# Kernel optimization log

Measured on AMD Instinct MI355X. Metric: run time of the kernel, lower is better.

## Reference

```python
import jax, jax.numpy as jnp
import numpy as np

D = 512
NHEAD = 8
BLOCK = 256
N = 131072
DFF = 2 * D
EPS = 1e-5


def _layernorm(x, g, b):
    mu = jnp.mean(x, axis=-1, keepdims=True)
    var = jnp.mean((x - mu) ** 2, axis=-1, keepdims=True)
    return (x - mu) * jax.lax.rsqrt(var + EPS) * g + b


def setup_inputs() -> dict:
    key = jax.random.key(0)
    ks = jax.random.split(key, 6)
    s = 0.02
    return {
        "x": jax.random.normal(ks[0], (N, D), jnp.float32),
        "in_proj_w": jax.random.normal(ks[1], (3 * D, D), jnp.float32) * s,
        "in_proj_b": jnp.zeros((3 * D,), jnp.float32),
        "out_w": jax.random.normal(ks[2], (D, D), jnp.float32) * s,
        "out_b": jnp.zeros((D,), jnp.float32),
        "lin1_w": jax.random.normal(ks[3], (DFF, D), jnp.float32) * s,
        "lin1_b": jnp.zeros((DFF,), jnp.float32),
        "lin2_w": jax.random.normal(ks[4], (D, DFF), jnp.float32) * s,
        "lin2_b": jnp.zeros((D,), jnp.float32),
        "ln1_g": jnp.ones((D,), jnp.float32),
        "ln1_beta": jnp.zeros((D,), jnp.float32),
        "ln2_g": jnp.ones((D,), jnp.float32),
        "ln2_beta": jnp.zeros((D,), jnp.float32),
        "block_size": BLOCK,
    }


def reference(x, in_proj_w, in_proj_b, out_w, out_b, lin1_w, lin1_b,
              lin2_w, lin2_b, ln1_g, ln1_beta, ln2_g, ln2_beta, block_size):
    n, d = x.shape
    nb = n // block_size  # N divisible by block_size -> equal chunks
    hd = d // NHEAD
    xb = x.reshape(nb, block_size, d)  # [B,S,D], each block independent

    # --- Multi-head self-attention (per block, batched) ---
    qkv = jnp.einsum('bsd,ed->bse', xb, in_proj_w) + in_proj_b  # [B,S,3D]
    q, k, v = jnp.split(qkv, 3, axis=-1)
    q = q.reshape(nb, block_size, NHEAD, hd)
    k = k.reshape(nb, block_size, NHEAD, hd)
    v = v.reshape(nb, block_size, NHEAD, hd)
    scores = jnp.einsum('bshd,bthd->bhst', q, k) / jnp.sqrt(jnp.float32(hd))
    probs = jax.nn.softmax(scores, axis=-1)
    ctx = jnp.einsum('bhst,bthd->bshd', probs, v).reshape(nb, block_size, d)
    attn_out = jnp.einsum('bsd,ed->bse', ctx, out_w) + out_b

    # post-norm residuals (torch default norm_first=False)
    h = _layernorm(xb + attn_out, ln1_g, ln1_beta)

    # --- FFN with exact-erf gelu ---
    ff = jnp.einsum('bsd,fd->bsf', h, lin1_w) + lin1_b
    ff = jax.nn.gelu(ff, approximate=False)
    ff = jnp.einsum('bsf,df->bsd', ff, lin2_w) + lin2_b
    out = _layernorm(h + ff, ln2_g, ln2_beta)
    return out.reshape(n, d)
```

## Files before the change

kernel.cpp:

```cpp
#include <hip/hip_runtime.h>
#include <hip/hip_bf16.h>
#include <math.h>

#define NTOK 131072
#define DMODEL 512
#define DFF_ 1024
#define NHEAD 8
#define HD 64
#define BLK 256
#define NB (NTOK / BLK)

typedef __hip_bfloat16 bf16;

__device__ __forceinline__ float bf_to_f(unsigned short u) {
    return __uint_as_float(((unsigned)u) << 16);
}
__device__ __forceinline__ unsigned short f_to_bf(float f) {
    bf16 h = __float2bfloat16(f);
    return __builtin_bit_cast(unsigned short, h);
}

typedef __bf16 bfrag __attribute__((ext_vector_type(8)));
typedef float f4t __attribute__((ext_vector_type(4)));

__device__ __forceinline__ float loadR(const float* p) { return *p; }
__device__ __forceinline__ float loadR(const ushort* p) { return bf_to_f(*p); }
__device__ __forceinline__ void storeC(float* p, float v) { *p = v; }
__device__ __forceinline__ void storeC(ushort* p, float v) { *p = f_to_bf(v); }

#define GLD_LDS(g, l)                                        \
    __builtin_amdgcn_global_load_lds(                        \
        (const __attribute__((address_space(1))) void*)(g),  \
        (__attribute__((address_space(3))) void*)(l), 16, 0, 0)

template <typename TO, typename TR, bool RESID, bool DO_GELU>
__global__ __launch_bounds__(256) void gemm_bf16(const ushort* __restrict__ A,
                                                 const ushort* __restrict__ B,
                                                 const float* __restrict__ bias,
                                                 const TR* __restrict__ resid,
                                                 TO* __restrict__ C,
                                                 int M, int Nn, int K) {
    __shared__ __align__(16) ushort As[128 * 64];
    __shared__ __align__(16) ushort Bs[128 * 64];

    const int tid = threadIdx.x;
    const int lane = tid & 63;
    const int w = tid >> 6;
    const int wm = w >> 1, wn = w & 1;

    const int ntn = Nn >> 7;
    int wg = blockIdx.x;
    const int cpx = (int)gridDim.x >> 3;
    wg = (wg & 7) * cpx + (wg >> 3);
    const int m0 = (wg / ntn) << 7;
    const int n0 = (wg % ntn) << 7;

    const int lr8 = lane >> 3;
    const int gsc = (lane & 7) << 3;

    const ushort* pa[4];
    const ushort* pb[4];
    ushort* la[4];
    ushort* lb[4];
#pragma unroll
    for (int i = 0; i < 4; ++i) {
        const int chunk = (w << 2) + i;
        const int r = (chunk << 3) + lr8;
        pa[i] = A + (size_t)(m0 + r) * K + gsc;
        pb[i] = B + (size_t)(n0 + r) * K + gsc;
        la[i] = As + (chunk << 9);
        lb[i] = Bs + (chunk << 9);
    }

    f4t zz = {0.f, 0.f, 0.f, 0.f};
    f4t acc[4][4];
#pragma unroll
    for (int i = 0; i < 4; ++i)
#pragma unroll
        for (int j = 0; j < 4; ++j) acc[i][j] = zz;

    const int fr = lane & 15;
    const int kq = lane >> 4;

    for (int kt = 0; kt < K; kt += 64) {
#pragma unroll
        for (int i = 0; i < 4; ++i) {
            GLD_LDS(pa[i], la[i]);
            GLD_LDS(pb[i], lb[i]);
            pa[i] += 64;
            pb[i] += 64;
        }
        __syncthreads();
#pragma unroll
        for (int ks = 0; ks < 2; ++ks) {
            const int sg = ((ks << 2) + kq) << 3;
            bfrag av[4], bv[4];
#pragma unroll
            for (int f = 0; f < 4; ++f) {
                av[f] = *(const bfrag*)(As + (((wm << 6) + (f << 4) + fr) << 6) + sg);
                bv[f] = *(const bfrag*)(Bs + (((wn << 6) + (f << 4) + fr) << 6) + sg);
            }
#pragma unroll
            for (int fm = 0; fm < 4; ++fm)
#pragma unroll
                for (int fn = 0; fn < 4; ++fn)
                    acc[fm][fn] = __builtin_amdgcn_mfma_f32_16x16x32_bf16(
                        av[fm], bv[fn], acc[fm][fn], 0, 0, 0);
        }
        __syncthreads();
    }

#pragma unroll
    for (int fn = 0; fn < 4; ++fn) {
        const int col = n0 + (wn << 6) + (fn << 4) + fr;
        const float bs = bias[col];
#pragma unroll
        for (int fm = 0; fm < 4; ++fm) {
            const int rw = m0 + (wm << 6) + (fm << 4) + (kq << 2);
#pragma unroll
            for (int j = 0; j < 4; ++j) {
                float v = acc[fm][fn][j] + bs;
                const size_t off = (size_t)(rw + j) * Nn + col;
                if constexpr (RESID) v += loadR(resid + off);
                if constexpr (DO_GELU)
                    v = 0.5f * v * (1.f + erff(v * 0.70710678118654752f));
                storeC(C + off, v);
            }
        }
    }
}

__global__ __launch_bounds__(256, 1) void attn_mfma(const ushort* __restrict__ qkv,
                                                    ushort* __restrict__ ctx) {
    __shared__ __align__(16) ushort Ks[256][72];
    __shared__ __align__(16) ushort Vt[64][264];
    __shared__ __align__(16) ushort Pl[4][64][40];
    const int b = blockIdx.x >> 3;
    const int h = blockIdx.x & 7;
    const int t = threadIdx.x;
    const int lane = t & 63;
    const int w = t >> 6;
    const int fr = lane & 15;
    const int kq = lane >> 4;

    {
        const ushort* rowp = qkv + (size_t)(b * BLK + t) * 1536 + h * HD;
#pragma unroll
        for (int c = 0; c < 8; ++c) {
            uint4 kv = *(const uint4*)(rowp + DMODEL + c * 8);
            *(uint4*)&Ks[t][c * 8] = kv;
            union { uint4 u; ushort s[8]; } vv;
            vv.u = *(const uint4*)(rowp + 2 * DMODEL + c * 8);
#pragma unroll
            for (int e = 0; e < 8; ++e) Vt[c * 8 + e][t] = vv.s[e];
        }
    }

    bfrag qb[4][2];
#pragma unroll
    for (int fn = 0; fn < 4; ++fn) {
        const ushort* qp =
            qkv + (size_t)(b * BLK + (w << 6) + (fn << 4) + fr) * 1536 + h * HD;
#pragma unroll
        for (int ks = 0; ks < 2; ++ks)
            qb[fn][ks] = *(const bfrag*)(qp + (ks << 5) + (kq << 3));
    }
    __syncthreads();

    f4t zz = {0.f, 0.f, 0.f, 0.f};
    f4t o[4][4];
#pragma unroll
    for (int i = 0; i < 4; ++i)
#pragma unroll
        for (int j = 0; j < 4; ++j) o[i][j] = zz;
    float m[4] = {-1e30f, -1e30f, -1e30f, -1e30f};
    float l[4] = {0.f, 0.f, 0.f, 0.f};

    for (int kt = 0; kt < 4; ++kt) {
        f4t s[4][4];
#pragma unroll
        for (int i = 0; i < 4; ++i)
#pragma unroll
            for (int j = 0; j < 4; ++j) s[i][j] = zz;
#pragma unroll
        for (int ks = 0; ks < 2; ++ks) {
            bfrag ka[4];
#pragma unroll
            for (int fm = 0; fm < 4; ++fm)
                ka[fm] = *(const bfrag*)&Ks[(kt << 6) + (fm << 4) + fr][(ks << 5) + (kq << 3)];
#pragma unroll
            for (int fm = 0; fm < 4; ++fm)
#pragma unroll
                for (int fn = 0; fn < 4; ++fn)
                    s[fm][fn] = __builtin_amdgcn_mfma_f32_16x16x32_bf16(
                        ka[fm], qb[fn][ks], s[fm][fn], 0, 0, 0);
        }
#pragma unroll
        for (int fn = 0; fn < 4; ++fn) {
            float mx = -1e30f;
#pragma unroll
            for (int fm = 0; fm < 4; ++fm)
#pragma unroll
                for (int j = 0; j < 4; ++j) {
                    float v = s[fm][fn][j] * 0.125f;
                    s[fm][fn][j] = v;
                    mx = fmaxf(mx, v);
                }
            mx = fmaxf(mx, __shfl_xor(mx, 16));
            mx = fmaxf(mx, __shfl_xor(mx, 32));
            const float mn = fmaxf(m[fn], mx);
            const float corr = __expf(m[fn] - mn);
            m[fn] = mn;
            l[fn] *= corr;
#pragma unroll
            for (int fm = 0; fm < 4; ++fm)
#pragma unroll
                for (int j = 0; j < 4; ++j) o[fm][fn][j] *= corr;
            float ps = 0.f;
#pragma unroll
            for (int fm = 0; fm < 4; ++fm)
#pragma unroll
                for (int j = 0; j < 4; ++j) {
                    float p = __expf(s[fm][fn][j] - mn);
                    s[fm][fn][j] = p;
                    ps += p;
                }
            l[fn] += ps;
        }
#pragma unroll
        for (int fn = 0; fn < 4; ++fn)
#pragma unroll
            for (int fm = 0; fm < 4; ++fm)
#pragma unroll
                for (int jj = 0; jj < 2; ++jj) {
                    unsigned u = (unsigned)f_to_bf(s[fm][fn][2 * jj]) |
                                 ((unsigned)f_to_bf(s[fm][fn][2 * jj + 1]) << 16);
                    *(unsigned*)&Pl[w][(fn << 4) + fr][(fm << 4) + (kq << 2) + 2 * jj] = u;
                }
#pragma unroll
        for (int c = 0; c < 2; ++c) {
            bfrag va[4], pb[4];
#pragma unroll
            for (int fm = 0; fm < 4; ++fm)
                va[fm] = *(const bfrag*)&Vt[(fm << 4) + fr][(kt << 6) + (c << 5) + (kq << 3)];
#pragma unroll
            for (int fn = 0; fn < 4; ++fn)
                pb[fn] = *(const bfrag*)&Pl[w][(fn << 4) + fr][(c << 5) + (kq << 3)];
#pragma unroll
            for (int fm = 0; fm < 4; ++fm)
#pragma unroll
                for (int fn = 0; fn < 4; ++fn)
                    o[fm][fn] = __builtin_amdgcn_mfma_f32_16x16x32_bf16(
                        va[fm], pb[fn], o[fm][fn], 0, 0, 0);
        }
    }

    float linv[4];
#pragma unroll
    for (int fn = 0; fn < 4; ++fn) {
        float ls = l[fn];
        ls += __shfl_xor(ls, 16);
        ls += __shfl_xor(ls, 32);
        linv[fn] = 1.f / ls;
    }
#pragma unroll
    for (int fn = 0; fn < 4; ++fn) {
        const size_t qg = (size_t)(b * BLK + (w << 6) + (fn << 4) + fr);
#pragma unroll
        for (int fm = 0; fm < 4; ++fm) {
            ushort4 ov;
            ov.x = f_to_bf(o[fm][fn][0] * linv[fn]);
            ov.y = f_to_bf(o[fm][fn][1] * linv[fn]);
            ov.z = f_to_bf(o[fm][fn][2] * linv[fn]);
            ov.w = f_to_bf(o[fm][fn][3] * linv[fn]);
            *(ushort4*)(ctx + qg * DMODEL + h * HD + (fm << 4) + (kq << 2)) = ov;
        }
    }
}

template <bool WF, bool WB>
__global__ __launch_bounds__(256) void ln_rows2(const float* __restrict__ in,
                                                float* __restrict__ outf,
                                                ushort* __restrict__ outb,
                                                const float* __restrict__ gg,
                                                const float* __restrict__ bb) {
    const int lane = threadIdx.x & 63;
    const int wv = threadIdx.x >> 6;
    const size_t row = (size_t)blockIdx.x * 4 + wv;
    const float* p = in + row * DMODEL + lane * 8;
    float4 a = ((const float4*)p)[0];
    float4 c = ((const float4*)p)[1];
    float s = a.x + a.y + a.z + a.w + c.x + c.y + c.z + c.w;
    float ss = a.x * a.x + a.y * a.y + a.z * a.z + a.w * a.w +
               c.x * c.x + c.y * c.y + c.z * c.z + c.w * c.w;
#pragma unroll
    for (int off = 1; off < 64; off <<= 1) {
        s += __shfl_xor(s, off, 64);
        ss += __shfl_xor(ss, off, 64);
    }
    const float mu = s * (1.f / 512.f);
    const float var = ss * (1.f / 512.f) - mu * mu;
    const float rstd = 1.f / sqrtf(var + 1e-5f);
    const int c0 = lane * 8;
    float4 g0 = *(const float4*)(gg + c0), g1 = *(const float4*)(gg + c0 + 4);
    float4 b0 = *(const float4*)(bb + c0), b1 = *(const float4*)(bb + c0 + 4);
    float4 o0, o1;
    o0.x = (a.x - mu) * rstd * g0.x + b0.x;
    o0.y = (a.y - mu) * rstd * g0.y + b0.y;
    o0.z = (a.z - mu) * rstd * g0.z + b0.z;
    o0.w = (a.w - mu) * rstd * g0.w + b0.w;
    o1.x = (c.x - mu) * rstd * g1.x + b1.x;
    o1.y = (c.y - mu) * rstd * g1.y + b1.y;
    o1.z = (c.z - mu) * rstd * g1.z + b1.z;
    o1.w = (c.w - mu) * rstd * g1.w + b1.w;
    if constexpr (WF) {
        float* qp = outf + row * DMODEL + c0;
        ((float4*)qp)[0] = o0;
        ((float4*)qp)[1] = o1;
    }
    if constexpr (WB) {
        ushort* bp = outb + row * DMODEL + c0;
        ushort4 u0, u1;
        u0.x = f_to_bf(o0.x); u0.y = f_to_bf(o0.y);
        u0.z = f_to_bf(o0.z); u0.w = f_to_bf(o0.w);
        u1.x = f_to_bf(o1.x); u1.y = f_to_bf(o1.y);
        u1.z = f_to_bf(o1.z); u1.w = f_to_bf(o1.w);
        ((ushort4*)bp)[0] = u0;
        ((ushort4*)bp)[1] = u1;
    }
}

__global__ __launch_bounds__(256) void cvt_f32_bf16(const float* __restrict__ in,
                                                    ushort* __restrict__ out,
                                                    int n4) {
    int i = blockIdx.x * 256 + threadIdx.x;
    const int stride = gridDim.x * 256;
    for (; i < n4; i += stride) {
        float4 v = ((const float4*)in)[i];
        ushort4 o;
        o.x = f_to_bf(v.x); o.y = f_to_bf(v.y);
        o.z = f_to_bf(v.z); o.w = f_to_bf(v.w);
        ((ushort4*)out)[i] = o;
    }
}

extern "C" void kernel_launch(void* const* d_in, const int* in_sizes, int n_in,
                              void* d_out, int out_size, void* d_ws, size_t ws_size,
                              hipStream_t stream) {
    const float* x    = (const float*)d_in[0];
    const float* wqkv = (const float*)d_in[1];
    const float* bqkv = (const float*)d_in[2];
    const float* wo   = (const float*)d_in[3];
    const float* bo   = (const float*)d_in[4];
    const float* w1   = (const float*)d_in[5];
    const float* b1   = (const float*)d_in[6];
    const float* w2   = (const float*)d_in[7];
    const float* b2   = (const float*)d_in[8];
    const float* g1   = (const float*)d_in[9];
    const float* be1  = (const float*)d_in[10];
    const float* g2   = (const float*)d_in[11];
    const float* be2  = (const float*)d_in[12];
    float* out = (float*)d_out;

    const size_t MiB = 1ull << 20;
    char* ws = (char*)d_ws;
    char* ob = (char*)d_out;
    const bool roomy = ws_size >= 520 * MiB;

    ushort* qkv = (ushort*)ws;
    float*  h   = (float*)ws;
    ushort* hb  = (ushort*)(ws + 256 * MiB);
    ushort* ctx = (ushort*)ob;

    ushort *wqkvb, *wob, *w1b, *w2b, *xb, *ff;
    float* y2;
    if (roomy) {
        wqkvb = (ushort*)(ws + 512 * MiB);
        wob   = (ushort*)(ws + 514 * MiB);
        w1b   = (ushort*)(ws + 515 * MiB);
        w2b   = (ushort*)(ws + 516 * MiB);
        xb    = (ushort*)(ws + 384 * MiB);
        ff    = (ushort*)ob;
        y2    = (float*)(ws + 256 * MiB);
    } else {
        wqkvb = (ushort*)(ws + 384 * MiB);
        wob   = (ushort*)(ws + 386 * MiB);
        w1b   = (ushort*)(ws + 387 * MiB);
        w2b   = (ushort*)(ws + 388 * MiB);
        xb    = (ushort*)ob;
        ff    = (ushort*)ws;
        y2    = (float*)ob;
    }

    dim3 blk(256);
    auto cvt = [&](const float* src, ushort* dst, size_t n) {
        int n4 = (int)(n >> 2);
        int nb = (n4 + 255) / 256;
        if (nb > 4096) nb = 4096;
        cvt_f32_bf16<<<dim3(nb), blk, 0, stream>>>(src, dst, n4);
    };
    cvt(x, xb, (size_t)NTOK * DMODEL);
    cvt(wqkv, wqkvb, 1536 * 512);
    cvt(wo, wob, 512 * 512);
    cvt(w1, w1b, 1024 * 512);
    cvt(w2, w2b, 512 * 1024);

    gemm_bf16<ushort, float, false, false><<<dim3(12 * 1024), blk, 0, stream>>>(
        xb, wqkvb, bqkv, (const float*)nullptr, qkv, NTOK, 1536, 512);
    attn_mfma<<<dim3(NB * NHEAD), blk, 0, stream>>>(qkv, ctx);
    gemm_bf16<float, float, true, false><<<dim3(4 * 1024), blk, 0, stream>>>(
        ctx, wob, bo, x, h, NTOK, 512, 512);
    if (roomy)
        ln_rows2<true, true><<<dim3(NTOK / 4), blk, 0, stream>>>(h, h, hb, g1, be1);
    else
        ln_rows2<false, true><<<dim3(NTOK / 4), blk, 0, stream>>>(h, nullptr, hb, g1, be1);
    gemm_bf16<ushort, float, false, true><<<dim3(8 * 1024), blk, 0, stream>>>(
        hb, w1b, b1, (const float*)nullptr, ff, NTOK, 1024, 512);
    if (roomy)
        gemm_bf16<float, float, true, false><<<dim3(4 * 1024), blk, 0, stream>>>(
            ff, w2b, b2, h, y2, NTOK, 512, 1024);
    else
        gemm_bf16<float, ushort, true, false><<<dim3(4 * 1024), blk, 0, stream>>>(
            ff, w2b, b2, hb, y2, NTOK, 512, 1024);
    ln_rows2<true, false><<<dim3(NTOK / 4), blk, 0, stream>>>(y2, out, nullptr, g2, be2);
}
```

Before: 2.150 ms.

## Replace GEMM with 256x256 tiles, double-buffered LDS and XOR-swizzled loads

The bf16 GEMM becomes a 512-thread, 256x256-tile kernel. Global-to-LDS loads for the next K tile are double-buffered and interleaved with MFMA work, using explicit waitcnt and barriers, raised wave priority around the MFMAs, and an XOR swizzle on the LDS layout to avoid bank conflicts. The host side drops the workspace-size branch and always uses the compact buffer layout, so the second residual is read from the bf16 h copy. The larger tiles increase register and LDS use per block, which can cap occupancy.

Result: faster. 1.808 ms (-15.9%).

```diff
diff --git a/kernel.cpp b/kernel.cpp
--- a/kernel.cpp
+++ b/kernel.cpp
@@ -34,80 +34,97 @@
         (__attribute__((address_space(3))) void*)(l), 16, 0, 0)
 
 template <typename TO, typename TR, bool RESID, bool DO_GELU>
-__global__ __launch_bounds__(256) void gemm_bf16(const ushort* __restrict__ A,
+__global__ __launch_bounds__(512, 2) void gemm8p(const ushort* __restrict__ A,
                                                  const ushort* __restrict__ B,
                                                  const float* __restrict__ bias,
                                                  const TR* __restrict__ resid,
                                                  TO* __restrict__ C,
                                                  int M, int Nn, int K) {
-    __shared__ __align__(16) ushort As[128 * 64];
-    __shared__ __align__(16) ushort Bs[128 * 64];
+    __shared__ __align__(16) ushort Ls[2][2][2][128][64];
 
     const int tid = threadIdx.x;
     const int lane = tid & 63;
     const int w = tid >> 6;
-    const int wm = w >> 1, wn = w & 1;
-
-    const int ntn = Nn >> 7;
+    const int wm = w >> 2;
+    const int wn = w & 3;
+    const int fr = lane & 15;
+    const int kq = lane >> 4;
+    const int sr = lane >> 3;
+    const int su = (lane & 7) ^ sr;
+
+    const int ntn = Nn >> 8;
     int wg = blockIdx.x;
     const int cpx = (int)gridDim.x >> 3;
     wg = (wg & 7) * cpx + (wg >> 3);
-    const int m0 = (wg / ntn) << 7;
-    const int n0 = (wg % ntn) << 7;
-
-    const int lr8 = lane >> 3;
-    const int gsc = (lane & 7) << 3;
-
-    const ushort* pa[4];
-    const ushort* pb[4];
-    ushort* la[4];
-    ushort* lb[4];
-#pragma unroll
-    for (int i = 0; i < 4; ++i) {
-        const int chunk = (w << 2) + i;
-        const int r = (chunk << 3) + lr8;
-        pa[i] = A + (size_t)(m0 + r) * K + gsc;
-        pb[i] = B + (size_t)(n0 + r) * K + gsc;
-        la[i] = As + (chunk << 9);
-        lb[i] = Bs + (chunk << 9);
-    }
+    const int m0 = (wg / ntn) << 8;
+    const int n0 = (wg % ntn) << 8;
+
+    auto stage_ht = [&](int db, int mat, int t, int h) {
+#pragma unroll
+        for (int i = 0; i < 2; ++i) {
+            const int seg = (w << 1) + i;
+            const int rr = (h << 7) + (seg << 3) + sr;
+            const ushort* gp = (mat ? B : A) +
+                (size_t)((mat ? n0 : m0) + rr) * K + (t << 6) + (su << 3);
+            GLD_LDS(gp, &Ls[db][mat][h][seg << 3][0]);
+        }
+    };
 
     f4t zz = {0.f, 0.f, 0.f, 0.f};
-    f4t acc[4][4];
-#pragma unroll
-    for (int i = 0; i < 4; ++i)
+    f4t acc[8][4];
+#pragma unroll
+    for (int i = 0; i < 8; ++i)
 #pragma unroll
         for (int j = 0; j < 4; ++j) acc[i][j] = zz;
 
-    const int fr = lane & 15;
-    const int kq = lane >> 4;
-
-    for (int kt = 0; kt < K; kt += 64) {
-#pragma unroll
-        for (int i = 0; i < 4; ++i) {
-            GLD_LDS(pa[i], la[i]);
-            GLD_LDS(pb[i], lb[i]);
-            pa[i] += 64;
-            pb[i] += 64;
-        }
-        __syncthreads();
-#pragma unroll
-        for (int ks = 0; ks < 2; ++ks) {
-            const int sg = ((ks << 2) + kq) << 3;
+    const int NT = K >> 6;
+    stage_ht(0, 0, 0, 0); stage_ht(0, 0, 0, 1);
+    stage_ht(0, 1, 0, 0); stage_ht(0, 1, 0, 1);
+
+    for (int tt = 0; tt < NT; tt += 2) {
+#pragma unroll
+        for (int p = 0; p < 8; ++p) {
+            const int hi = p >> 2;
+            const int q = p & 3;
+            const int mh = q & 1;
+            const int ks = q >> 1;
+            const int dc = hi;
+            const int ds_ = 1 - hi;
+            const int st = tt + 1 + hi;
+            const bool do_stage = st < NT;
+
+            if (q == 0) {
+                if (do_stage) {
+                    stage_ht(ds_, 0, st, 0);
+                    asm volatile("s_waitcnt vmcnt(2)\n\ts_barrier" ::: "memory");
+                } else {
+                    asm volatile("s_waitcnt vmcnt(0)\n\ts_barrier" ::: "memory");
+                }
+            }
+
             bfrag av[4], bv[4];
+            const int uu = ((((ks << 2) | kq)) ^ (fr & 7)) << 3;
 #pragma unroll
             for (int f = 0; f < 4; ++f) {
-                av[f] = *(const bfrag*)(As + (((wm << 6) + (f << 4) + fr) << 6) + sg);
-                bv[f] = *(const bfrag*)(Bs + (((wn << 6) + (f << 4) + fr) << 6) + sg);
+                const int rA = (wm << 7) + (mh << 6) + (f << 4) + fr;
+                av[f] = *(const bfrag*)&Ls[dc][0][rA >> 7][rA & 127][uu];
+                const int rB = (wn << 6) + (f << 4) + fr;
+                bv[f] = *(const bfrag*)&Ls[dc][1][rB >> 7][rB & 127][uu];
             }
-#pragma unroll
-            for (int fm = 0; fm < 4; ++fm)
+            if (q != 0 && do_stage) {
+                stage_ht(ds_, q >> 1, st, q & 1);
+            }
+
+            __builtin_amdgcn_s_setprio(1);
+#pragma unroll
+            for (int f = 0; f < 4; ++f)
 #pragma unroll
                 for (int fn = 0; fn < 4; ++fn)
-                    acc[fm][fn] = __builtin_amdgcn_mfma_f32_16x16x32_bf16(
-                        av[fm], bv[fn], acc[fm][fn], 0, 0, 0);
-        }
-        __syncthreads();
+                    acc[(mh << 2) + f][fn] = __builtin_amdgcn_mfma_f32_16x16x32_bf16(
+                        av[f], bv[fn], acc[(mh << 2) + f][fn], 0, 0, 0);
+            __builtin_amdgcn_s_setprio(0);
+            __builtin_amdgcn_s_barrier();
+        }
     }
 
 #pragma unroll
@@ -115,8 +132,8 @@
         const int col = n0 + (wn << 6) + (fn << 4) + fr;
         const float bs = bias[col];
 #pragma unroll
-        for (int fm = 0; fm < 4; ++fm) {
-            const int rw = m0 + (wm << 6) + (fm << 4) + (kq << 2);
+        for (int fm = 0; fm < 8; ++fm) {
+            const int rw = m0 + (wm << 7) + (fm << 4) + (kq << 2);
 #pragma unroll
             for (int j = 0; j < 4; ++j) {
                 float v = acc[fm][fn][j] + bs;
@@ -365,39 +382,25 @@
     const size_t MiB = 1ull << 20;
     char* ws = (char*)d_ws;
     char* ob = (char*)d_out;
-    const bool roomy = ws_size >= 520 * MiB;
-
-    ushort* qkv = (ushort*)ws;
-    float*  h   = (float*)ws;
-    ushort* hb  = (ushort*)(ws + 256 * MiB);
-    ushort* ctx = (ushort*)ob;
-
-    ushort *wqkvb, *wob, *w1b, *w2b, *xb, *ff;
-    float* y2;
-    if (roomy) {
-        wqkvb = (ushort*)(ws + 512 * MiB);
-        wob   = (ushort*)(ws + 514 * MiB);
-        w1b   = (ushort*)(ws + 515 * MiB);
-        w2b   = (ushort*)(ws + 516 * MiB);
-        xb    = (ushort*)(ws + 384 * MiB);
-        ff    = (ushort*)ob;
-        y2    = (float*)(ws + 256 * MiB);
-    } else {
-        wqkvb = (ushort*)(ws + 384 * MiB);
-        wob   = (ushort*)(ws + 386 * MiB);
-        w1b   = (ushort*)(ws + 387 * MiB);
-        w2b   = (ushort*)(ws + 388 * MiB);
-        xb    = (ushort*)ob;
-        ff    = (ushort*)ws;
-        y2    = (float*)ob;
-    }
-
-    dim3 blk(256);
+
+    ushort* qkv   = (ushort*)ws;
+    float*  h     = (float*)ws;
+    float*  y2    = (float*)ws;
+    ushort* hb    = (ushort*)(ws + 256 * MiB);
+    ushort* wqkvb = (ushort*)(ws + 384 * MiB);
+    ushort* wob   = (ushort*)(ws + 386 * MiB);
+    ushort* w1b   = (ushort*)(ws + 387 * MiB);
+    ushort* w2b   = (ushort*)(ws + 388 * MiB);
+    ushort* xb    = (ushort*)ob;
+    ushort* ctx   = (ushort*)(ob + 128 * MiB);
+    ushort* ff    = (ushort*)ob;
+
+    dim3 b256(256), b512(512);
     auto cvt = [&](const float* src, ushort* dst, size_t n) {
         int n4 = (int)(n >> 2);
         int nb = (n4 + 255) / 256;
         if (nb > 4096) nb = 4096;
-        cvt_f32_bf16<<<dim3(nb), blk, 0, stream>>>(src, dst, n4);
+        cvt_f32_bf16<<<dim3(nb), b256, 0, stream>>>(src, dst, n4);
     };
     cvt(x, xb, (size_t)NTOK * DMODEL);
     cvt(wqkv, wqkvb, 1536 * 512);
@@ -405,22 +408,15 @@
     cvt(w1, w1b, 1024 * 512);
     cvt(w2, w2b, 512 * 1024);
 
-    gemm_bf16<ushort, float, false, false><<<dim3(12 * 1024), blk, 0, stream>>>(
+    gemm8p<ushort, float, false, false><<<dim3(512 * 6), b512, 0, stream>>>(
         xb, wqkvb, bqkv, (const float*)nullptr, qkv, NTOK, 1536, 512);
-    attn_mfma<<<dim3(NB * NHEAD), blk, 0, stream>>>(qkv, ctx);
-    gemm_bf16<float, float, true, false><<<dim3(4 * 1024), blk, 0, stream>>>(
+    attn_mfma<<<dim3(NB * NHEAD), b256, 0, stream>>>(qkv, ctx);
+    gemm8p<float, float, true, false><<<dim3(512 * 2), b512, 0, stream>>>(
         ctx, wob, bo, x, h, NTOK, 512, 512);
-    if (roomy)
-        ln_rows2<true, true><<<dim3(NTOK / 4), blk, 0, stream>>>(h, h, hb, g1, be1);
-    else
-        ln_rows2<false, true><<<dim3(NTOK / 4), blk, 0, stream>>>(h, nullptr, hb, g1, be1);
-    gemm_bf16<ushort, float, false, true><<<dim3(8 * 1024), blk, 0, stream>>>(
+    ln_rows2<false, true><<<dim3(NTOK / 4), b256, 0, stream>>>(h, nullptr, hb, g1, be1);
+    gemm8p<ushort, float, false, true><<<dim3(512 * 4), b512, 0, stream>>>(
         hb, w1b, b1, (const float*)nullptr, ff, NTOK, 1024, 512);
-    if (roomy)
-        gemm_bf16<float, float, true, false><<<dim3(4 * 1024), blk, 0, stream>>>(
-            ff, w2b, b2, h, y2, NTOK, 512, 1024);
-    else
-        gemm_bf16<float, ushort, true, false><<<dim3(4 * 1024), blk, 0, stream>>>(
-            ff, w2b, b2, hb, y2, NTOK, 512, 1024);
-    ln_rows2<true, false><<<dim3(NTOK / 4), blk, 0, stream>>>(y2, out, nullptr, g2, be2);
-}
+    gemm8p<float, ushort, true, false><<<dim3(512 * 2), b512, 0, stream>>>(
+        ff, w2b, b2, hb, y2, NTOK, 512, 1024);
+    ln_rows2<true, false><<<dim3(NTOK / 4), b256, 0, stream>>>(y2, out, nullptr, g2, be2);
+}
```
